# Kernel tuning notes

Hardware: AMD Instinct MI355X
Metric: run time of the kernel (lower is better)

The kernel has to match this reference:

```python
import jax, jax.numpy as jnp
import numpy as np

N = 100000           # nodes
E = 1600000          # edges (no self loops; added inside reference)
IN_DIM = 128
H1, C1 = 8, 16       # layer-1 heads, per-head channels (concat -> 128)
H2, C2 = 1, 40       # layer-2 heads, out channels (concat=False)


def setup_inputs() -> dict:
    key = jax.random.key(0)
    ks = jax.random.split(key, 10)
    x = jax.random.normal(ks[0], (N, IN_DIM), jnp.float32)
    src = jax.random.randint(ks[1], (E,), 0, N, dtype=jnp.int32)
    dst = jax.random.randint(ks[2], (E,), 0, N, dtype=jnp.int32)
    dst = jnp.where(dst == src, (dst + 1) % N, dst)  # emulate remove_self_loops
    edge_index = jnp.stack([src, dst], axis=0)
    sc = 0.05
    return {
        "x": x,
        "edge_index": edge_index,
        "W1": jax.random.normal(ks[3], (H1 * C1, IN_DIM), jnp.float32) * sc,
        "b1": jnp.zeros((H1 * C1,), jnp.float32),
        "att1": jax.random.normal(ks[4], (H1, 2 * C1), jnp.float32) * sc,
        "bias1": jnp.zeros((H1 * C1,), jnp.float32),
        "W2": jax.random.normal(ks[5], (H2 * C2, H1 * C1), jnp.float32) * sc,
        "b2": jnp.zeros((H2 * C2,), jnp.float32),
        "att2": jax.random.normal(ks[6], (H2, 2 * C2), jnp.float32) * sc,
        "bias2": jnp.zeros((C2,), jnp.float32),
    }


def _gat_layer(x, src, dst, W, b, att, bias, H, C, concat):
    n = x.shape[0]
    # add self loops (inputs are guaranteed self-loop free)
    loop = jnp.arange(n, dtype=src.dtype)
    s = jnp.concatenate([src, loop])
    d = jnp.concatenate([dst, loop])
    h = (x @ W.T + b).reshape(n, H, C)            # [N,H,C]
    # per-node halves of cat([x_i, x_j]) . att  -> gather scalars per edge
    a_i = jnp.einsum('nhc,hc->nh', h, att[:, :C])  # dst half
    a_j = jnp.einsum('nhc,hc->nh', h, att[:, C:])  # src half
    e = jax.nn.leaky_relu(a_i[d] + a_j[s], negative_slope=0.2)  # [Etot,H]
    # segment softmax over destination nodes (pyg_utils.softmax)
    m = jax.ops.segment_max(e, d, num_segments=n)
    ex = jnp.exp(e - m[d])
    denom = jax.ops.segment_sum(ex, d, num_segments=n)
    alpha = ex / (denom[d] + 1e-16)
    msg = h[s] * alpha[:, :, None]                # [Etot,H,C]
    out = jax.ops.segment_sum(msg.reshape(-1, H * C), d, num_segments=n)
    if not concat:
        out = out.reshape(n, H, C).mean(axis=1)
    return out + bias


def reference(x, edge_index, W1, b1, att1, bias1, W2, b2, att2, bias2):
    src, dst = edge_index[0], edge_index[1]
    h = _gat_layer(x, src, dst, W1, b1, att1, bias1, H1, C1, True)
    h = jax.nn.elu(h)  # dropout p=0 / eval -> no-op
    h = _gat_layer(h, src, dst, W2, b2, att2, bias2, H2, C2, False)
    return jax.nn.log_softmax(h, axis=1)
```

## Files before the change

### kernel.cpp

```cpp
#include <hip/hip_runtime.h>
#include <hip/hip_fp16.h>
#include <math.h>


typedef _Float16 f16x8 __attribute__((ext_vector_type(8)));
typedef float f32x4 __attribute__((ext_vector_type(4)));
typedef float f32x2 __attribute__((ext_vector_type(2)));

__device__ __forceinline__ float lrelu02(float x){ return x > 0.f ? x : 0.2f*x; }
__device__ __forceinline__ unsigned char f2fp8(float v){
  return (unsigned char)(__builtin_amdgcn_cvt_pk_fp8_f32(v, v, 0, false) & 0xff);
}

#define BSHIFT 7
#define BMASK  127
#define SPLIT_CHUNK 4096

__global__ void k_initcur(int* __restrict__ gcur, int nbucket, int cap){
  int b = blockIdx.x*blockDim.x + threadIdx.x;
  if (b < nbucket) gcur[b*16] = b*cap;
}

__global__ __launch_bounds__(256) void k_split(const int* __restrict__ src,
    const int* __restrict__ dst, int* __restrict__ gcur, int* __restrict__ tmp,
    int E, int nbucket){
  __shared__ int hist[1024];
  int tid = threadIdx.x;
  for (int t = tid; t < 1024; t += 256) hist[t] = 0;
  __syncthreads();
  int lo = blockIdx.x*SPLIT_CHUNK;
  int ds[16], ss[16];
  #pragma unroll
  for (int k = 0; k < 16; ++k){
    int i = lo + tid + k*256;
    bool p = i < E;
    ds[k] = p ? dst[i] : 0;
    ss[k] = p ? src[i] : 0;
    if (p) atomicAdd(&hist[ds[k] >> BSHIFT], 1);
  }
  __syncthreads();
  for (int b = tid; b < nbucket; b += 256){
    int c = hist[b];
    if (c) hist[b] = atomicAdd(&gcur[b*16], c);
  }
  __syncthreads();
  #pragma unroll
  for (int k = 0; k < 16; ++k){
    int i = lo + tid + k*256;
    if (i < E){
      int r = atomicAdd(&hist[ds[k] >> BSHIFT], 1);
      tmp[r] = ss[k] | ((ds[k] & BMASK) << 17);
    }
  }
}

__global__ void k_bscan(const int* __restrict__ gcur, int* __restrict__ bstart,
                        int* __restrict__ rowstart, int nbucket, int cap, int E, int N){
  __shared__ int lds[256];
  int t = threadIdx.x;
  int v[4]; int s = 0;
  #pragma unroll
  for (int k = 0; k < 4; ++k){
    int idx = t*4 + k;
    v[k] = (idx < nbucket) ? (gcur[idx*16] - idx*cap) : 0;
    s += v[k];
  }
  lds[t] = s;
  __syncthreads();
  for (int off = 1; off < 256; off <<= 1){
    int x = (t >= off) ? lds[t-off] : 0;
    __syncthreads();
    lds[t] += x;
    __syncthreads();
  }
  int run = (t == 0) ? 0 : lds[t-1];
  #pragma unroll
  for (int k = 0; k < 4; ++k){
    int idx = t*4 + k;
    if (idx < nbucket) bstart[idx] = run;
    run += v[k];
  }
  if (t == 0){ bstart[nbucket] = E; rowstart[N] = E; }
}

__global__ __launch_bounds__(256) void k_final(const int* __restrict__ tmp,
    const int* __restrict__ gcur, const int* __restrict__ bstart,
    int* __restrict__ rowstart, int* __restrict__ csr, int cap, int N){
  __shared__ int h[128];
  __shared__ int sc[128];
  __shared__ int cur[128];
  int b = blockIdx.x;
  int tid = threadIdx.x;
  int cnt  = gcur[b*16] - b*cap;
  int base = bstart[b];
  if (tid < 128) h[tid] = 0;
  __syncthreads();
  const int* tb = tmp + (size_t)b*cap;
  for (int i = tid; i < cnt; i += 256) atomicAdd(&h[tb[i] >> 17], 1);
  __syncthreads();
  if (tid < 128) sc[tid] = h[tid];
  __syncthreads();
  for (int off = 1; off < 128; off <<= 1){
    int x = (tid < 128 && tid >= off) ? sc[tid-off] : 0;
    __syncthreads();
    if (tid < 128) sc[tid] += x;
    __syncthreads();
  }
  if (tid < 128){
    int excl = sc[tid] - h[tid];
    int node = b*128 + tid;
    if (node < N) rowstart[node] = base + excl;
    cur[tid] = base + excl;
  }
  __syncthreads();
  for (int i = tid; i < cnt; i += 256){
    int v = tb[i];
    int p = atomicAdd(&cur[v >> 17], 1);
    csr[p] = v & 0x1FFFF;
  }
}

__global__ void k_prep(const float* __restrict__ W1, const float* __restrict__ b1,
                       const float* __restrict__ att1,
                       const float* __restrict__ W2, const float* __restrict__ b2,
                       const float* __restrict__ att2,
                       _Float16* __restrict__ W1h, _Float16* __restrict__ W2h,
                       _Float16* __restrict__ attB1, _Float16* __restrict__ attB2,
                       float* __restrict__ consts){
  int i = blockIdx.x*blockDim.x + threadIdx.x;
  if (i < 16384){ W1h[i] = (_Float16)W1[i]; return; }
  i -= 16384;
  if (i < 6144){ int r = i >> 7; W2h[i] = (r < 40)? (_Float16)W2[i] : (_Float16)0.f; return; }
  i -= 6144;
  if (i < 2048){
    int j = i >> 7, k = i & 127;
    int h = j & 7, half = (j >> 3)*16;
    float s = 0.f;
    for (int c = 0; c < 16; ++c) s += att1[h*32 + half + c]*W1[(h*16+c)*128 + k];
    attB1[i] = (_Float16)s; return;
  }
  i -= 2048;
  if (i < 2048){
    int j = i >> 7, k = i & 127;
    float s = 0.f;
    if (j < 2){ const float* av = att2 + j*40; for (int c = 0; c < 40; ++c) s += av[c]*W2[c*128 + k]; }
    attB2[i] = (_Float16)s; return;
  }
  i -= 2048;
  if (i < 18){
    float s = 0.f;
    if (i < 8){ for (int c = 0; c < 16; ++c) s += b1[i*16+c]*att1[i*32+c]; }
    else if (i < 16){ int h = i-8; for (int c = 0; c < 16; ++c) s += b1[h*16+c]*att1[h*32+16+c]; }
    else if (i == 16){ for (int c = 0; c < 40; ++c) s += b2[c]*att2[c]; }
    else { for (int c = 0; c < 40; ++c) s += b2[c]*att2[40+c]; }
    consts[i] = s;
  }
}

__global__ __launch_bounds__(256) void k_gemm1(const float* __restrict__ x,
    const _Float16* __restrict__ Wh, const _Float16* __restrict__ attB,
    const float* __restrict__ b1, const float* __restrict__ consts,
    unsigned char* __restrict__ h1f8, float* __restrict__ a1i, float* __restrict__ a1j, int N){
  int wid  = (blockIdx.x*256 + threadIdx.x) >> 6;
  int lane = threadIdx.x & 63;
  int m0 = wid*16;
  if (m0 >= N) return;
  int col = lane & 15, quad = lane >> 4;
  const float* xr = x + (size_t)(m0+col)*128 + quad*8;
  f32x4 acc[9];
  #pragma unroll
  for (int t=0;t<9;t++){ acc[t][0]=0.f; acc[t][1]=0.f; acc[t][2]=0.f; acc[t][3]=0.f; }
  #pragma unroll
  for (int q=0;q<4;q++){
    float4 f0 = ((const float4*)(xr + q*32))[0];
    float4 f1 = ((const float4*)(xr + q*32))[1];
    f16x8 a;
    a[0]=(_Float16)f0.x; a[1]=(_Float16)f0.y; a[2]=(_Float16)f0.z; a[3]=(_Float16)f0.w;
    a[4]=(_Float16)f1.x; a[5]=(_Float16)f1.y; a[6]=(_Float16)f1.z; a[7]=(_Float16)f1.w;
    #pragma unroll
    for (int t=0;t<8;t++){
      const f16x8* Bp = (const f16x8*)(Wh + (size_t)(t*16+col)*128 + q*32 + quad*8);
      acc[t] = __builtin_amdgcn_mfma_f32_16x16x32_f16(a, *Bp, acc[t], 0,0,0);
    }
    const f16x8* Ap = (const f16x8*)(attB + (size_t)col*128 + q*32 + quad*8);
    acc[8] = __builtin_amdgcn_mfma_f32_16x16x32_f16(a, *Ap, acc[8], 0,0,0);
  }
  #pragma unroll
  for (int t=0;t<8;t++){
    int c = t*16 + col;
    float bb = b1[c];
    #pragma unroll
    for (int r=0;r<4;r++){
      h1f8[(size_t)(m0 + quad*4 + r)*128 + c] = f2fp8(acc[t][r] + bb);
    }
  }
  float hb = consts[col];
  #pragma unroll
  for (int r=0;r<4;r++){
    int node = m0 + quad*4 + r;
    float v = acc[8][r] + hb;
    if (col < 8) a1i[node*8 + col] = v;
    else         a1j[node*8 + (col-8)] = v;
  }
}

__global__ __launch_bounds__(256) void k_agg1(const uint2* __restrict__ h1q,
    const float* __restrict__ a1i, const float* __restrict__ a1j,
    const int* __restrict__ rowstart, const int* __restrict__ csr,
    const float* __restrict__ bias, uint4* __restrict__ x2u4, int N){
  int lane = threadIdx.x & 63;
  int n = (blockIdx.x*blockDim.x + threadIdx.x) >> 6;
  if (n >= N) return;
  int ql = lane & 15, qt = lane >> 4;
  unsigned hd = (unsigned)ql >> 1;
  int rs = rowstart[n], re = rowstart[n+1];
  float ai2 = a1i[(unsigned)n*8u + hd];
  float a0=0.f,a1=0.f,a2=0.f,a3=0.f,a4=0.f,a5=0.f,a6=0.f,a7=0.f,den=0.f;
  {
    float w = (qt==0)? __expf(lrelu02(ai2 + a1j[(unsigned)n*8u + hd])) : 0.f;
    uint2 u = h1q[(unsigned)n*16u + (unsigned)ql];
    f32x2 f0 = __builtin_amdgcn_cvt_pk_f32_fp8((int)u.x, false);
    f32x2 f1 = __builtin_amdgcn_cvt_pk_f32_fp8((int)u.x, true);
    f32x2 f2 = __builtin_amdgcn_cvt_pk_f32_fp8((int)u.y, false);
    f32x2 f3 = __builtin_amdgcn_cvt_pk_f32_fp8((int)u.y, true);
    a0=w*f0[0]; a1=w*f0[1]; a2=w*f1[0]; a3=w*f1[1];
    a4=w*f2[0]; a5=w*f2[1]; a6=w*f3[0]; a7=w*f3[1];
    den = w;
  }
  int last = re - 1;
  if (rs < re){
    unsigned cs0 = (unsigned)csr[min(rs+ 0+qt,last)];
    unsigned cs1 = (unsigned)csr[min(rs+ 4+qt,last)];
    unsigned cs2 = (unsigned)csr[min(rs+ 8+qt,last)];
    unsigned cs3 = (unsigned)csr[min(rs+12+qt,last)];
    unsigned cs4 = (unsigned)csr[min(rs+16+qt,last)];
    unsigned cs5 = (unsigned)csr[min(rs+20+qt,last)];
    unsigned cs6 = (unsigned)csr[min(rs+24+qt,last)];
    unsigned cs7 = (unsigned)csr[min(rs+28+qt,last)];
    float aj0 = a1j[cs0*8u+hd], aj1 = a1j[cs1*8u+hd];
    float aj2 = a1j[cs2*8u+hd], aj3 = a1j[cs3*8u+hd];
    float aj4 = a1j[cs4*8u+hd], aj5 = a1j[cs5*8u+hd];
    float aj6 = a1j[cs6*8u+hd], aj7 = a1j[cs7*8u+hd];
    uint2 u0 = h1q[(size_t)cs0*16u + (unsigned)ql];
    uint2 u1 = h1q[(size_t)cs1*16u + (unsigned)ql];
    uint2 u2 = h1q[(size_t)cs2*16u + (unsigned)ql];
    uint2 u3 = h1q[(size_t)cs3*16u + (unsigned)ql];
    int e0 = rs;

#define AGG1_ST(US, CF, CS, AJ, OFF)                                         \
    {                                                                        \
      uint2 cur = US;                                                        \
      US = h1q[(size_t)CF*16u + (unsigned)ql];                               \
      unsigned nc = (unsigned)csr[min(e0+OFF+32+qt, last)];                  \
      float w = (e0+OFF+qt < re)? __expf(lrelu02(ai2 + AJ)) : 0.f;           \
      den += w;                                                              \
      f32x2 g0 = __builtin_amdgcn_cvt_pk_f32_fp8((int)cur.x, false);         \
      f32x2 g1 = __builtin_amdgcn_cvt_pk_f32_fp8((int)cur.x, true);          \
      f32x2 g2 = __builtin_amdgcn_cvt_pk_f32_fp8((int)cur.y, false);         \
      f32x2 g3 = __builtin_amdgcn_cvt_pk_f32_fp8((int)cur.y, true);          \
      a0 += w*g0[0]; a1 += w*g0[1]; a2 += w*g1[0]; a3 += w*g1[1];            \
      a4 += w*g2[0]; a5 += w*g2[1]; a6 += w*g3[0]; a7 += w*g3[1];            \
      CS = nc; AJ = a1j[nc*8u + hd];                                         \
    }

    while (e0 < re){
      AGG1_ST(u0, cs4, cs0, aj0, 0)
      if (e0+4 >= re) break;
      AGG1_ST(u1, cs5, cs1, aj1, 4)
      if (e0+8 >= re) break;
      AGG1_ST(u2, cs6, cs2, aj2, 8)
      if (e0+12 >= re) break;
      AGG1_ST(u3, cs7, cs3, aj3, 12)
      if (e0+16 >= re) break;
      AGG1_ST(u0, cs0, cs4, aj4, 16)
      if (e0+20 >= re) break;
      AGG1_ST(u1, cs1, cs5, aj5, 20)
      if (e0+24 >= re) break;
      AGG1_ST(u2, cs2, cs6, aj6, 24)
      if (e0+28 >= re) break;
      AGG1_ST(u3, cs3, cs7, aj7, 28)
      e0 += 32;
    }
#undef AGG1_ST
  }
  #pragma unroll
  for (int off = 16; off < 64; off <<= 1){
    den += __shfl_xor(den, off);
    a0 += __shfl_xor(a0, off); a1 += __shfl_xor(a1, off);
    a2 += __shfl_xor(a2, off); a3 += __shfl_xor(a3, off);
    a4 += __shfl_xor(a4, off); a5 += __shfl_xor(a5, off);
    a6 += __shfl_xor(a6, off); a7 += __shfl_xor(a7, off);
  }
  if (qt == 0){
    float invd = 1.f/(den + 1e-16f);
    const float4* b4 = (const float4*)(bias + 8*ql);
    float4 bl = b4[0], bh = b4[1];
    float o0=a0*invd+bl.x, o1=a1*invd+bl.y, o2=a2*invd+bl.z, o3=a3*invd+bl.w;
    float o4=a4*invd+bh.x, o5=a5*invd+bh.y, o6=a6*invd+bh.z, o7=a7*invd+bh.w;
    o0=(o0>0.f)?o0:(__expf(o0)-1.f); o1=(o1>0.f)?o1:(__expf(o1)-1.f);
    o2=(o2>0.f)?o2:(__expf(o2)-1.f); o3=(o3>0.f)?o3:(__expf(o3)-1.f);
    o4=(o4>0.f)?o4:(__expf(o4)-1.f); o5=(o5>0.f)?o5:(__expf(o5)-1.f);
    o6=(o6>0.f)?o6:(__expf(o6)-1.f); o7=(o7>0.f)?o7:(__expf(o7)-1.f);
    __half2 p0 = __floats2half2_rn(o0,o1), p1 = __floats2half2_rn(o2,o3);
    __half2 p2 = __floats2half2_rn(o4,o5), p3 = __floats2half2_rn(o6,o7);
    uint4 o;
    o.x = *(unsigned*)&p0; o.y = *(unsigned*)&p1; o.z = *(unsigned*)&p2; o.w = *(unsigned*)&p3;
    x2u4[(unsigned)n*16u + (unsigned)ql] = o;
  }
}

__global__ __launch_bounds__(256) void k_gemm2(const _Float16* __restrict__ xh,
    const _Float16* __restrict__ Wh, const _Float16* __restrict__ attB,
    const float* __restrict__ b2, const float* __restrict__ consts,
    unsigned char* __restrict__ h2f8, float* __restrict__ a2i, float* __restrict__ a2j, int N){
  int wid  = (blockIdx.x*256 + threadIdx.x) >> 6;
  int lane = threadIdx.x & 63;
  int m0 = wid*16;
  if (m0 >= N) return;
  int col = lane & 15, quad = lane >> 4;
  const f16x8* A8 = (const f16x8*)(xh + (size_t)(m0+col)*128 + quad*8);
  f32x4 acc[4];
  #pragma unroll
  for (int t=0;t<4;t++){ acc[t][0]=0.f; acc[t][1]=0.f; acc[t][2]=0.f; acc[t][3]=0.f; }
  #pragma unroll
  for (int q=0;q<4;q++){
    f16x8 a = A8[q*4];
    #pragma unroll
    for (int t=0;t<3;t++){
      const f16x8* Bp = (const f16x8*)(Wh + (size_t)(t*16+col)*128 + q*32 + quad*8);
      acc[t] = __builtin_amdgcn_mfma_f32_16x16x32_f16(a, *Bp, acc[t], 0,0,0);
    }
    const f16x8* Bp2 = (const f16x8*)(attB + (size_t)col*128 + q*32 + quad*8);
    acc[3] = __builtin_amdgcn_mfma_f32_16x16x32_f16(a, *Bp2, acc[3], 0,0,0);
  }
  #pragma unroll
  for (int t=0;t<3;t++){
    int c = t*16 + col;
    if (c < 40){
      float bb = b2[c];
      #pragma unroll
// ... 15 lines not shown

__global__ __launch_bounds__(256) void k_agg2(const unsigned* __restrict__ h2u,
    const float* __restrict__ a2i, const float* __restrict__ a2j,
    const int* __restrict__ rowstart, const int* __restrict__ csr,
    const float* __restrict__ bias, float* __restrict__ out, int N){
  int lane = threadIdx.x & 63;
  int wid = (blockIdx.x*blockDim.x + threadIdx.x) >> 6;
  int qt = lane >> 4, ql = lane & 15;
  int n = wid*4 + qt;
  if (n >= N) return;
  bool act = ql < 10;
  unsigned cl = act ? (unsigned)ql : 0u;
  int rs = rowstart[n], re = rowstart[n+1];
  float ai = a2i[n];
  float wself = __expf(lrelu02(ai + a2j[n]));
  float a0,a1,a2,a3,den;
  {
    unsigned u = h2u[(unsigned)n*10u + cl];
    f32x2 f0 = __builtin_amdgcn_cvt_pk_f32_fp8((int)u, false);
    f32x2 f1 = __builtin_amdgcn_cvt_pk_f32_fp8((int)u, true);
    a0 = wself*f0[0]; a1 = wself*f0[1]; a2 = wself*f1[0]; a3 = wself*f1[1];
    den = wself;
  }
  if (rs < re){
    int last = re - 1;
    unsigned cs0 = (unsigned)csr[min(rs+0,last)];
    unsigned cs1 = (unsigned)csr[min(rs+1,last)];
    unsigned cs2 = (unsigned)csr[min(rs+2,last)];
    unsigned cs3 = (unsigned)csr[min(rs+3,last)];
    unsigned cs4 = (unsigned)csr[min(rs+4,last)];
    unsigned cs5 = (unsigned)csr[min(rs+5,last)];
    unsigned cs6 = (unsigned)csr[min(rs+6,last)];
    unsigned cs7 = (unsigned)csr[min(rs+7,last)];
    float aj0 = a2j[cs0], aj1 = a2j[cs1], aj2 = a2j[cs2], aj3 = a2j[cs3];
    float aj4 = a2j[cs4], aj5 = a2j[cs5], aj6 = a2j[cs6], aj7 = a2j[cs7];
    unsigned u0 = h2u[cs0*10u + cl];
    unsigned u1 = h2u[cs1*10u + cl];
    unsigned u2 = h2u[cs2*10u + cl];
    unsigned u3 = h2u[cs3*10u + cl];
    int e0 = rs;

#define AGG2_ST(US, CF, CS, AJ, OFF)                                         \
    {                                                                        \
      unsigned cur = US;                                                     \
      US = h2u[CF*10u + cl];                                                 \
      unsigned nc = (unsigned)csr[min(e0+OFF+8, last)];                      \
      float w = (e0+OFF < re)? __expf(lrelu02(ai + AJ)) : 0.f;               \
      den += w;                                                              \
      f32x2 g0 = __builtin_amdgcn_cvt_pk_f32_fp8((int)cur, false);           \
      f32x2 g1 = __builtin_amdgcn_cvt_pk_f32_fp8((int)cur, true);            \
      a0 += w*g0[0]; a1 += w*g0[1]; a2 += w*g1[0]; a3 += w*g1[1];            \
      CS = nc; AJ = a2j[nc];                                                 \
    }

    while (e0 < re){
      AGG2_ST(u0, cs4, cs0, aj0, 0)
      AGG2_ST(u1, cs5, cs1, aj1, 1)
      AGG2_ST(u2, cs6, cs2, aj2, 2)
      AGG2_ST(u3, cs7, cs3, aj3, 3)
      AGG2_ST(u0, cs0, cs4, aj4, 4)
      AGG2_ST(u1, cs1, cs5, aj5, 5)
      AGG2_ST(u2, cs2, cs6, aj6, 6)
      AGG2_ST(u3, cs3, cs7, aj7, 7)
      e0 += 8;
    }
#undef AGG2_ST
  }
  float invd = 1.f/(den + 1e-16f);
  const float4* b4 = (const float4*)(bias + 4*cl);
  float4 bb = b4[0];
  float v0 = a0*invd + bb.x, v1 = a1*invd + bb.y;
  float v2 = a2*invd + bb.z, v3 = a3*invd + bb.w;
  float mv = act ? fmaxf(fmaxf(v0,v1), fmaxf(v2,v3)) : -INFINITY;
  #pragma unroll
  for (int off = 1; off < 16; off <<= 1) mv = fmaxf(mv, __shfl_xor(mv, off));
  float se = act ? (__expf(v0-mv)+__expf(v1-mv)+__expf(v2-mv)+__expf(v3-mv)) : 0.f;
  #pragma unroll
  for (int off = 1; off < 16; off <<= 1) se += __shfl_xor(se, off);
  float ls = __logf(se);
  if (act){
    float4 o = make_float4(v0-mv-ls, v1-mv-ls, v2-mv-ls, v3-mv-ls);
    ((float4*)out)[(unsigned)n*10u + cl] = o;
  }
}

// ... 15 lines not shown
  const int* src = ei;
  const int* dst = ei + E;

  char* ws = (char*)d_ws;
  size_t off = 0;
  auto alloc = [&](size_t bytes)->char*{
    char* p = ws + off; off += (bytes + 255) & ~(size_t)255; return p;
  };
  unsigned char* h1f8 = (unsigned char*)alloc((size_t)N*128);
  _Float16*      x2h  = (_Float16*)alloc((size_t)N*128*2);
  unsigned char* h2f8 = (unsigned char*)alloc((size_t)N*40);
  float* a1i  = (float*)alloc((size_t)N*8*4);
  float* a1j  = (float*)alloc((size_t)N*8*4);
  float* a2i  = (float*)alloc((size_t)N*4);
  float* a2j  = (float*)alloc((size_t)N*4);
  _Float16* W1h   = (_Float16*)alloc(16384*2);
  _Float16* W2h   = (_Float16*)alloc(6144*2);
  _Float16* attB1 = (_Float16*)alloc(2048*2);
  _Float16* attB2 = (_Float16*)alloc(2048*2);
  float* consts = (float*)alloc(18*4);
  int*   rowst = (int*)  alloc((size_t)(N+1)*4);
  int*   csr   = (int*)  alloc((size_t)E*4);

  int nbucket = (N + BMASK) >> BSHIFT;
  int meanb = (E + nbucket - 1)/nbucket;
  int cap = ((2*meanb + 1023)/1024)*1024;
  if (cap < 2048) cap = 2048;

  int*   gcur   = (int*)alloc((size_t)nbucket*64);
  int*   bstart = (int*)alloc((size_t)(nbucket+1)*4);
  int*   tmp    = (int*)x2h;

  int nchunk = (E + SPLIT_CHUNK - 1)/SPLIT_CHUNK;
  k_initcur<<<(nbucket+255)/256, 256, 0, stream>>>(gcur, nbucket, cap);
  k_split<<<nchunk, 256, 0, stream>>>(src, dst, gcur, tmp, E, nbucket);
  k_bscan<<<1, 256, 0, stream>>>(gcur, bstart, rowst, nbucket, cap, E, N);
  k_final<<<nbucket, 256, 0, stream>>>(tmp, gcur, bstart, rowst, csr, cap, N);
  k_prep<<<105, 256, 0, stream>>>(W1, b1, att1, W2, b2, att2, W1h, W2h, attB1, attB2, consts);

  int gblk = ((N+15)/16 + 3)/4;
  k_gemm1<<<gblk, 256, 0, stream>>>(x, W1h, attB1, b1, consts, h1f8, a1i, a1j, N);
  k_agg1<<<(N*64+255)/256, 256, 0, stream>>>((const uint2*)h1f8, a1i, a1j, rowst, csr, bias1, (uint4*)x2h, N);

  k_gemm2<<<gblk, 256, 0, stream>>>(x2h, W2h, attB2, b2, consts, h2f8, a2i, a2j, N);
  k_agg2<<<(N+15)/16, 256, 0, stream>>>((const unsigned*)h2f8, a2i, a2j, rowst, csr, bias2, (float*)d_out, N);
}
```

Measured before the change: 315.5 us.

## Fuse edge bucketing with layer-1 GEMM and widen agg1 lanes to 16 channels

The edge split (CSR bucketing) and the layer-1 GEMM now run as one horizontally fused kernel, with block index deciding which body runs. The init kernel is replaced by a memset, so bucket counters now start at zero and the bucket offset is added at use. Separately, agg1 is remapped so each lane handles 16 fp8 channels with uint4 loads and 8 edges are processed in parallel per wavefront instead of 4. This cuts launch count and lets independent work overlap, and halves gather instructions per edge. The cost is more registers per lane in agg1 and one more shuffle round in the reduction.

```diff
diff --git a/kernel.cpp b/kernel.cpp
--- a/kernel.cpp
+++ b/kernel.cpp
@@ -16,19 +16,14 @@
 #define BMASK  127
 #define SPLIT_CHUNK 4096
 
-__global__ void k_initcur(int* __restrict__ gcur, int nbucket, int cap){
-  int b = blockIdx.x*blockDim.x + threadIdx.x;
-  if (b < nbucket) gcur[b*16] = b*cap;
-}
-
-__global__ __launch_bounds__(256) void k_split(const int* __restrict__ src,
+__device__ __forceinline__ void split_body(int blk, const int* __restrict__ src,
     const int* __restrict__ dst, int* __restrict__ gcur, int* __restrict__ tmp,
-    int E, int nbucket){
+    int E, int nbucket, int cap){
   __shared__ int hist[1024];
   int tid = threadIdx.x;
   for (int t = tid; t < 1024; t += 256) hist[t] = 0;
   __syncthreads();
-  int lo = blockIdx.x*SPLIT_CHUNK;
+  int lo = blk*SPLIT_CHUNK;
   int ds[16], ss[16];
   #pragma unroll
   for (int k = 0; k < 16; ++k){
@@ -41,7 +36,7 @@
   __syncthreads();
   for (int b = tid; b < nbucket; b += 256){
     int c = hist[b];
-    if (c) hist[b] = atomicAdd(&gcur[b*16], c);
+    if (c) hist[b] = b*cap + atomicAdd(&gcur[b*16], c);
   }
   __syncthreads();
   #pragma unroll
@@ -54,15 +49,75 @@
   }
 }
 
+__device__ __forceinline__ void gemm1_body(int gb, const float* __restrict__ x,
+    const _Float16* __restrict__ Wh, const _Float16* __restrict__ attB,
+    const float* __restrict__ b1, const float* __restrict__ consts,
+    unsigned char* __restrict__ h1f8, float* __restrict__ a1i, float* __restrict__ a1j, int N){
+  int wid  = (gb*256 + (int)threadIdx.x) >> 6;
+  int lane = threadIdx.x & 63;
+  int m0 = wid*16;
+  if (m0 >= N) return;
+  int col = lane & 15, quad = lane >> 4;
+  const float* xr = x + (size_t)(m0+col)*128 + quad*8;
+  f32x4 acc[9];
+  #pragma unroll
+  for (int t=0;t<9;t++){ acc[t][0]=0.f; acc[t][1]=0.f; acc[t][2]=0.f; acc[t][3]=0.f; }
+  #pragma unroll
+  for (int q=0;q<4;q++){
+    float4 f0 = ((const float4*)(xr + q*32))[0];
+    float4 f1 = ((const float4*)(xr + q*32))[1];
+    f16x8 a;
+    a[0]=(_Float16)f0.x; a[1]=(_Float16)f0.y; a[2]=(_Float16)f0.z; a[3]=(_Float16)f0.w;
+    a[4]=(_Float16)f1.x; a[5]=(_Float16)f1.y; a[6]=(_Float16)f1.z; a[7]=(_Float16)f1.w;
+    #pragma unroll
+    for (int t=0;t<8;t++){
+      const f16x8* Bp = (const f16x8*)(Wh + (size_t)(t*16+col)*128 + q*32 + quad*8);
+      acc[t] = __builtin_amdgcn_mfma_f32_16x16x32_f16(a, *Bp, acc[t], 0,0,0);
+    }
+    const f16x8* Ap = (const f16x8*)(attB + (size_t)col*128 + q*32 + quad*8);
+    acc[8] = __builtin_amdgcn_mfma_f32_16x16x32_f16(a, *Ap, acc[8], 0,0,0);
+  }
+  #pragma unroll
+  for (int t=0;t<8;t++){
+    int c = t*16 + col;
+    float bb = b1[c];
+    #pragma unroll
+    for (int r=0;r<4;r++){
+      h1f8[(size_t)(m0 + quad*4 + r)*128 + c] = f2fp8(acc[t][r] + bb);
+    }
+  }
+  float hb = consts[col];
+  #pragma unroll
+  for (int r=0;r<4;r++){
+    int node = m0 + quad*4 + r;
+    float v = acc[8][r] + hb;
+    if (col < 8) a1i[node*8 + col] = v;
+    else         a1j[node*8 + (col-8)] = v;
+  }
+}
+
+__global__ __launch_bounds__(256) void k_fused1(const int* __restrict__ src,
+    const int* __restrict__ dst, int* __restrict__ gcur, int* __restrict__ tmp,
+    int E, int nbucket, int nchunk, int cap,
+    const float* __restrict__ x, const _Float16* __restrict__ Wh,
+    const _Float16* __restrict__ attB, const float* __restrict__ b1,
+    const float* __restrict__ consts, unsigned char* __restrict__ h1f8,
+    float* __restrict__ a1i, float* __restrict__ a1j, int N){
+  if ((int)blockIdx.x < nchunk)
+    split_body(blockIdx.x, src, dst, gcur, tmp, E, nbucket, cap);
+  else
+    gemm1_body(blockIdx.x - nchunk, x, Wh, attB, b1, consts, h1f8, a1i, a1j, N);
+}
+
 __global__ void k_bscan(const int* __restrict__ gcur, int* __restrict__ bstart,
-                        int* __restrict__ rowstart, int nbucket, int cap, int E, int N){
+                        int* __restrict__ rowstart, int nbucket, int E, int N){
   __shared__ int lds[256];
   int t = threadIdx.x;
   int v[4]; int s = 0;
   #pragma unroll
   for (int k = 0; k < 4; ++k){
     int idx = t*4 + k;
-    v[k] = (idx < nbucket) ? (gcur[idx*16] - idx*cap) : 0;
+    v[k] = (idx < nbucket) ? gcur[idx*16] : 0;
     s += v[k];
   }
   lds[t] = s;
@@ -91,7 +146,7 @@
   __shared__ int cur[128];
   int b = blockIdx.x;
   int tid = threadIdx.x;
-  int cnt  = gcur[b*16] - b*cap;
+  int cnt  = gcur[b*16];
   int base = bstart[b];
   if (tid < 128) h[tid] = 0;
   __syncthreads();
@@ -157,155 +212,126 @@
   }
 }
 
-__global__ __launch_bounds__(256) void k_gemm1(const float* __restrict__ x,
-    const _Float16* __restrict__ Wh, const _Float16* __restrict__ attB,
-    const float* __restrict__ b1, const float* __restrict__ consts,
-    unsigned char* __restrict__ h1f8, float* __restrict__ a1i, float* __restrict__ a1j, int N){
-  int wid  = (blockIdx.x*256 + threadIdx.x) >> 6;
-  int lane = threadIdx.x & 63;
-  int m0 = wid*16;
-  if (m0 >= N) return;
-  int col = lane & 15, quad = lane >> 4;
-  const float* xr = x + (size_t)(m0+col)*128 + quad*8;
-  f32x4 acc[9];
-  #pragma unroll
-  for (int t=0;t<9;t++){ acc[t][0]=0.f; acc[t][1]=0.f; acc[t][2]=0.f; acc[t][3]=0.f; }
-  #pragma unroll
-  for (int q=0;q<4;q++){
-    float4 f0 = ((const float4*)(xr + q*32))[0];
-    float4 f1 = ((const float4*)(xr + q*32))[1];
-    f16x8 a;
-    a[0]=(_Float16)f0.x; a[1]=(_Float16)f0.y; a[2]=(_Float16)f0.z; a[3]=(_Float16)f0.w;
-    a[4]=(_Float16)f1.x; a[5]=(_Float16)f1.y; a[6]=(_Float16)f1.z; a[7]=(_Float16)f1.w;
-    #pragma unroll
-    for (int t=0;t<8;t++){
-      const f16x8* Bp = (const f16x8*)(Wh + (size_t)(t*16+col)*128 + q*32 + quad*8);
-      acc[t] = __builtin_amdgcn_mfma_f32_16x16x32_f16(a, *Bp, acc[t], 0,0,0);
-    }
-    const f16x8* Ap = (const f16x8*)(attB + (size_t)col*128 + q*32 + quad*8);
-    acc[8] = __builtin_amdgcn_mfma_f32_16x16x32_f16(a, *Ap, acc[8], 0,0,0);
-  }
-  #pragma unroll
-  for (int t=0;t<8;t++){
-    int c = t*16 + col;
-    float bb = b1[c];
-    #pragma unroll
-    for (int r=0;r<4;r++){
-      h1f8[(size_t)(m0 + quad*4 + r)*128 + c] = f2fp8(acc[t][r] + bb);
-    }
-  }
-  float hb = consts[col];
-  #pragma unroll
-  for (int r=0;r<4;r++){
-    int node = m0 + quad*4 + r;
-    float v = acc[8][r] + hb;
-    if (col < 8) a1i[node*8 + col] = v;
-    else         a1j[node*8 + (col-8)] = v;
-  }
-}
-
-__global__ __launch_bounds__(256) void k_agg1(const uint2* __restrict__ h1q,
+__global__ __launch_bounds__(256) void k_agg1(const uint4* __restrict__ h1q4,
     const float* __restrict__ a1i, const float* __restrict__ a1j,
     const int* __restrict__ rowstart, const int* __restrict__ csr,
     const float* __restrict__ bias, uint4* __restrict__ x2u4, int N){
   int lane = threadIdx.x & 63;
   int n = (blockIdx.x*blockDim.x + threadIdx.x) >> 6;
   if (n >= N) return;
-  int ql = lane & 15, qt = lane >> 4;
-  unsigned hd = (unsigned)ql >> 1;
+  int o = lane & 7, oct = lane >> 3;
   int rs = rowstart[n], re = rowstart[n+1];
-  float ai2 = a1i[(unsigned)n*8u + hd];
-  float a0=0.f,a1=0.f,a2=0.f,a3=0.f,a4=0.f,a5=0.f,a6=0.f,a7=0.f,den=0.f;
+  float ai2 = a1i[(unsigned)n*8u + (unsigned)o];
+  float s0=0.f,s1=0.f,s2=0.f,s3=0.f,s4=0.f,s5=0.f,s6=0.f,s7=0.f;
+  float s8=0.f,s9=0.f,s10=0.f,s11=0.f,s12=0.f,s13=0.f,s14=0.f,s15=0.f;
+  float den=0.f;
+
+#define ACC16(U, W)                                                          \
+  { f32x2 g;                                                                 \
+    g = __builtin_amdgcn_cvt_pk_f32_fp8((int)(U).x,false); s0 +=(W)*g[0]; s1 +=(W)*g[1]; \
+    g = __builtin_amdgcn_cvt_pk_f32_fp8((int)(U).x,true ); s2 +=(W)*g[0]; s3 +=(W)*g[1]; \
+    g = __builtin_amdgcn_cvt_pk_f32_fp8((int)(U).y,false); s4 +=(W)*g[0]; s5 +=(W)*g[1]; \
+    g = __builtin_amdgcn_cvt_pk_f32_fp8((int)(U).y,true ); s6 +=(W)*g[0]; s7 +=(W)*g[1]; \
+    g = __builtin_amdgcn_cvt_pk_f32_fp8((int)(U).z,false); s8 +=(W)*g[0]; s9 +=(W)*g[1]; \
+    g = __builtin_amdgcn_cvt_pk_f32_fp8((int)(U).z,true ); s10+=(W)*g[0]; s11+=(W)*g[1]; \
+    g = __builtin_amdgcn_cvt_pk_f32_fp8((int)(U).w,false); s12+=(W)*g[0]; s13+=(W)*g[1]; \
+    g = __builtin_amdgcn_cvt_pk_f32_fp8((int)(U).w,true ); s14+=(W)*g[0]; s15+=(W)*g[1]; }
+
   {
-    float w = (qt==0)? __expf(lrelu02(ai2 + a1j[(unsigned)n*8u + hd])) : 0.f;
-    uint2 u = h1q[(unsigned)n*16u + (unsigned)ql];
-    f32x2 f0 = __builtin_amdgcn_cvt_pk_f32_fp8((int)u.x, false);
-    f32x2 f1 = __builtin_amdgcn_cvt_pk_f32_fp8((int)u.x, true);
-    f32x2 f2 = __builtin_amdgcn_cvt_pk_f32_fp8((int)u.y, false);
-    f32x2 f3 = __builtin_amdgcn_cvt_pk_f32_fp8((int)u.y, true);
-    a0=w*f0[0]; a1=w*f0[1]; a2=w*f1[0]; a3=w*f1[1];
-    a4=w*f2[0]; a5=w*f2[1]; a6=w*f3[0]; a7=w*f3[1];
+    float w = (oct==0)? __expf(lrelu02(ai2 + a1j[(unsigned)n*8u + (unsigned)o])) : 0.f;
+    uint4 u = h1q4[(unsigned)n*8u + (unsigned)o];
+    ACC16(u, w)
     den = w;
   }
   int last = re - 1;
   if (rs < re){
-    unsigned cs0 = (unsigned)csr[min(rs+ 0+qt,last)];
-    unsigned cs1 = (unsigned)csr[min(rs+ 4+qt,last)];
-    unsigned cs2 = (unsigned)csr[min(rs+ 8+qt,last)];
-    unsigned cs3 = (unsigned)csr[min(rs+12+qt,last)];
-    unsigned cs4 = (unsigned)csr[min(rs+16+qt,last)];
-    unsigned cs5 = (unsigned)csr[min(rs+20+qt,last)];
-    unsigned cs6 = (unsigned)csr[min(rs+24+qt,last)];
-    unsigned cs7 = (unsigned)csr[min(rs+28+qt,last)];
-    float aj0 = a1j[cs0*8u+hd], aj1 = a1j[cs1*8u+hd];
-    float aj2 = a1j[cs2*8u+hd], aj3 = a1j[cs3*8u+hd];
-    float aj4 = a1j[cs4*8u+hd], aj5 = a1j[cs5*8u+hd];
-    float aj6 = a1j[cs6*8u+hd], aj7 = a1j[cs7*8u+hd];
-    uint2 u0 = h1q[(size_t)cs0*16u + (unsigned)ql];
-    uint2 u1 = h1q[(size_t)cs1*16u + (unsigned)ql];
-    uint2 u2 = h1q[(size_t)cs2*16u + (unsigned)ql];
-    uint2 u3 = h1q[(size_t)cs3*16u + (unsigned)ql];
+    unsigned cs0 = (unsigned)csr[min(rs+ 0+oct,last)];
+    unsigned cs1 = (unsigned)csr[min(rs+ 8+oct,last)];
+    unsigned cs2 = (unsigned)csr[min(rs+16+oct,last)];
+    unsigned cs3 = (unsigned)csr[min(rs+24+oct,last)];
+    unsigned cs4 = (unsigned)csr[min(rs+32+oct,last)];
+    unsigned cs5 = (unsigned)csr[min(rs+40+oct,last)];
+    unsigned cs6 = (unsigned)csr[min(rs+48+oct,last)];
+    unsigned cs7 = (unsigned)csr[min(rs+56+oct,last)];
+    float aj0 = a1j[cs0*8u+o], aj1 = a1j[cs1*8u+o];
+    float aj2 = a1j[cs2*8u+o], aj3 = a1j[cs3*8u+o];
+    float aj4 = a1j[cs4*8u+o], aj5 = a1j[cs5*8u+o];
+    float aj6 = a1j[cs6*8u+o], aj7 = a1j[cs7*8u+o];
+    uint4 u0 = h1q4[(size_t)cs0*8u + (unsigned)o];
+    uint4 u1 = h1q4[(size_t)cs1*8u + (unsigned)o];
+    uint4 u2 = h1q4[(size_t)cs2*8u + (unsigned)o];
+    uint4 u3 = h1q4[(size_t)cs3*8u + (unsigned)o];
     int e0 = rs;
 
 #define AGG1_ST(US, CF, CS, AJ, OFF)                                         \
     {                                                                        \
-      uint2 cur = US;                                                        \
-      US = h1q[(size_t)CF*16u + (unsigned)ql];                               \
-      unsigned nc = (unsigned)csr[min(e0+OFF+32+qt, last)];                  \
-      float w = (e0+OFF+qt < re)? __expf(lrelu02(ai2 + AJ)) : 0.f;           \
+      uint4 cur = US;                                                        \
+      US = h1q4[(size_t)CF*8u + (unsigned)o];                                \
+      unsigned nc = (unsigned)csr[min(e0+OFF+64+oct, last)];                 \
+      float w = (e0+OFF+oct < re)? __expf(lrelu02(ai2 + AJ)) : 0.f;          \
       den += w;                                                              \
-      f32x2 g0 = __builtin_amdgcn_cvt_pk_f32_fp8((int)cur.x, false);         \
-      f32x2 g1 = __builtin_amdgcn_cvt_pk_f32_fp8((int)cur.x, true);          \
-      f32x2 g2 = __builtin_amdgcn_cvt_pk_f32_fp8((int)cur.y, false);         \
-      f32x2 g3 = __builtin_amdgcn_cvt_pk_f32_fp8((int)cur.y, true);          \
-      a0 += w*g0[0]; a1 += w*g0[1]; a2 += w*g1[0]; a3 += w*g1[1];            \
-      a4 += w*g2[0]; a5 += w*g2[1]; a6 += w*g3[0]; a7 += w*g3[1];            \
-      CS = nc; AJ = a1j[nc*8u + hd];                                         \
+      ACC16(cur, w)                                                          \
+      CS = nc; AJ = a1j[nc*8u + (unsigned)o];                                \
     }
 
     while (e0 < re){
       AGG1_ST(u0, cs4, cs0, aj0, 0)
-      if (e0+4 >= re) break;
-      AGG1_ST(u1, cs5, cs1, aj1, 4)
       if (e0+8 >= re) break;
-      AGG1_ST(u2, cs6, cs2, aj2, 8)
-      if (e0+12 >= re) break;
-      AGG1_ST(u3, cs7, cs3, aj3, 12)
+      AGG1_ST(u1, cs5, cs1, aj1, 8)
       if (e0+16 >= re) break;
-      AGG1_ST(u0, cs0, cs4, aj4, 16)
-      if (e0+20 >= re) break;
-      AGG1_ST(u1, cs1, cs5, aj5, 20)
+      AGG1_ST(u2, cs6, cs2, aj2, 16)
       if (e0+24 >= re) break;
-      AGG1_ST(u2, cs2, cs6, aj6, 24)
-      if (e0+28 >= re) break;
-      AGG1_ST(u3, cs3, cs7, aj7, 28)
-      e0 += 32;
+      AGG1_ST(u3, cs7, cs3, aj3, 24)
+      if (e0+32 >= re) break;
+      AGG1_ST(u0, cs0, cs4, aj4, 32)
+      if (e0+40 >= re) break;
+      AGG1_ST(u1, cs1, cs5, aj5, 40)
+      if (e0+48 >= re) break;
+      AGG1_ST(u2, cs2, cs6, aj6, 48)
+      if (e0+56 >= re) break;
+      AGG1_ST(u3, cs3, cs7, aj7, 56)
+      e0 += 64;
     }
 #undef AGG1_ST
   }
-  #pragma unroll
-  for (int off = 16; off < 64; off <<= 1){
+#undef ACC16
+  #pragma unroll
+  for (int off = 8; off < 64; off <<= 1){
     den += __shfl_xor(den, off);
-    a0 += __shfl_xor(a0, off); a1 += __shfl_xor(a1, off);
-    a2 += __shfl_xor(a2, off); a3 += __shfl_xor(a3, off);
-    a4 += __shfl_xor(a4, off); a5 += __shfl_xor(a5, off);
-    a6 += __shfl_xor(a6, off); a7 += __shfl_xor(a7, off);
-  }
-  if (qt == 0){
+    s0 += __shfl_xor(s0, off);  s1 += __shfl_xor(s1, off);
+    s2 += __shfl_xor(s2, off);  s3 += __shfl_xor(s3, off);
+    s4 += __shfl_xor(s4, off);  s5 += __shfl_xor(s5, off);
+    s6 += __shfl_xor(s6, off);  s7 += __shfl_xor(s7, off);
+    s8 += __shfl_xor(s8, off);  s9 += __shfl_xor(s9, off);
+    s10+= __shfl_xor(s10,off);  s11+= __shfl_xor(s11,off);
+    s12+= __shfl_xor(s12,off);  s13+= __shfl_xor(s13,off);
+    s14+= __shfl_xor(s14,off);  s15+= __shfl_xor(s15,off);
+  }
+  if (oct == 0){
     float invd = 1.f/(den + 1e-16f);
-    const float4* b4 = (const float4*)(bias + 8*ql);
-    float4 bl = b4[0], bh = b4[1];
-    float o0=a0*invd+bl.x, o1=a1*invd+bl.y, o2=a2*invd+bl.z, o3=a3*invd+bl.w;
-    float o4=a4*invd+bh.x, o5=a5*invd+bh.y, o6=a6*invd+bh.z, o7=a7*invd+bh.w;
-    o0=(o0>0.f)?o0:(__expf(o0)-1.f); o1=(o1>0.f)?o1:(__expf(o1)-1.f);
-    o2=(o2>0.f)?o2:(__expf(o2)-1.f); o3=(o3>0.f)?o3:(__expf(o3)-1.f);
-    o4=(o4>0.f)?o4:(__expf(o4)-1.f); o5=(o5>0.f)?o5:(__expf(o5)-1.f);
-    o6=(o6>0.f)?o6:(__expf(o6)-1.f); o7=(o7>0.f)?o7:(__expf(o7)-1.f);
-    __half2 p0 = __floats2half2_rn(o0,o1), p1 = __floats2half2_rn(o2,o3);
-    __half2 p2 = __floats2half2_rn(o4,o5), p3 = __floats2half2_rn(o6,o7);
-    uint4 o;
-    o.x = *(unsigned*)&p0; o.y = *(unsigned*)&p1; o.z = *(unsigned*)&p2; o.w = *(unsigned*)&p3;
-    x2u4[(unsigned)n*16u + (unsigned)ql] = o;
+    const float4* b4 = (const float4*)(bias + 16*o);
+    float4 bb0 = b4[0], bb1 = b4[1], bb2 = b4[2], bb3 = b4[3];
+    float o0 =s0 *invd+bb0.x, o1 =s1 *invd+bb0.y, o2 =s2 *invd+bb0.z, o3 =s3 *invd+bb0.w;
+    float o4 =s4 *invd+bb1.x, o5 =s5 *invd+bb1.y, o6 =s6 *invd+bb1.z, o7 =s7 *invd+bb1.w;
+    float o8 =s8 *invd+bb2.x, o9 =s9 *invd+bb2.y, o10=s10*invd+bb2.z, o11=s11*invd+bb2.w;
+    float o12=s12*invd+bb3.x, o13=s13*invd+bb3.y, o14=s14*invd+bb3.z, o15=s15*invd+bb3.w;
+    o0 =(o0 >0.f)?o0 :(__expf(o0 )-1.f); o1 =(o1 >0.f)?o1 :(__expf(o1 )-1.f);
+    o2 =(o2 >0.f)?o2 :(__expf(o2 )-1.f); o3 =(o3 >0.f)?o3 :(__expf(o3 )-1.f);
+    o4 =(o4 >0.f)?o4 :(__expf(o4 )-1.f); o5 =(o5 >0.f)?o5 :(__expf(o5 )-1.f);
+    o6 =(o6 >0.f)?o6 :(__expf(o6 )-1.f); o7 =(o7 >0.f)?o7 :(__expf(o7 )-1.f);
+    o8 =(o8 >0.f)?o8 :(__expf(o8 )-1.f); o9 =(o9 >0.f)?o9 :(__expf(o9 )-1.f);
+    o10=(o10>0.f)?o10:(__expf(o10)-1.f); o11=(o11>0.f)?o11:(__expf(o11)-1.f);
+    o12=(o12>0.f)?o12:(__expf(o12)-1.f); o13=(o13>0.f)?o13:(__expf(o13)-1.f);
+    o14=(o14>0.f)?o14:(__expf(o14)-1.f); o15=(o15>0.f)?o15:(__expf(o15)-1.f);
+    __half2 p0 = __floats2half2_rn(o0 ,o1 ), p1 = __floats2half2_rn(o2 ,o3 );
+    __half2 p2 = __floats2half2_rn(o4 ,o5 ), p3 = __floats2half2_rn(o6 ,o7 );
+    __half2 p4 = __floats2half2_rn(o8 ,o9 ), p5 = __floats2half2_rn(o10,o11);
+    __half2 p6 = __floats2half2_rn(o12,o13), p7 = __floats2half2_rn(o14,o15);
+    uint4 w0, w1;
+    w0.x = *(unsigned*)&p0; w0.y = *(unsigned*)&p1; w0.z = *(unsigned*)&p2; w0.w = *(unsigned*)&p3;
+    w1.x = *(unsigned*)&p4; w1.y = *(unsigned*)&p5; w1.z = *(unsigned*)&p6; w1.w = *(unsigned*)&p7;
+    x2u4[(unsigned)n*16u + (unsigned)(o*2)    ] = w0;
+    x2u4[(unsigned)n*16u + (unsigned)(o*2 + 1)] = w1;
   }
 }
 
@@ -487,15 +513,16 @@
   int*   tmp    = (int*)x2h;
 
   int nchunk = (E + SPLIT_CHUNK - 1)/SPLIT_CHUNK;
-  k_initcur<<<(nbucket+255)/256, 256, 0, stream>>>(gcur, nbucket, cap);
-  k_split<<<nchunk, 256, 0, stream>>>(src, dst, gcur, tmp, E, nbucket);
-  k_bscan<<<1, 256, 0, stream>>>(gcur, bstart, rowst, nbucket, cap, E, N);
+  int gblk = ((N+15)/16 + 3)/4;
+
+  hipMemsetAsync(gcur, 0, (size_t)nbucket*64, stream);
+  k_prep<<<105, 256, 0, stream>>>(W1, b1, att1, W2, b2, att2, W1h, W2h, attB1, attB2, consts);
+  k_fused1<<<nchunk + gblk, 256, 0, stream>>>(src, dst, gcur, tmp, E, nbucket, nchunk, cap,
+                                              x, W1h, attB1, b1, consts, h1f8, a1i, a1j, N);
+  k_bscan<<<1, 256, 0, stream>>>(gcur, bstart, rowst, nbucket, E, N);
   k_final<<<nbucket, 256, 0, stream>>>(tmp, gcur, bstart, rowst, csr, cap, N);
-  k_prep<<<105, 256, 0, stream>>>(W1, b1, att1, W2, b2, att2, W1h, W2h, attB1, attB2, consts);
-
-  int gblk = ((N+15)/16 + 3)/4;
-  k_gemm1<<<gblk, 256, 0, stream>>>(x, W1h, attB1, b1, consts, h1f8, a1i, a1j, N);
-  k_agg1<<<(N*64+255)/256, 256, 0, stream>>>((const uint2*)h1f8, a1i, a1j, rowst, csr, bias1, (uint4*)x2h, N);
+
+  k_agg1<<<(N*64+255)/256, 256, 0, stream>>>((const uint4*)h1f8, a1i, a1j, rowst, csr, bias1, (uint4*)x2h, N);
 
   k_gemm2<<<gblk, 256, 0, stream>>>(x2h, W2h, attB2, b2, consts, h2f8, a2i, a2j, N);
   k_agg2<<<(N+15)/16, 256, 0, stream>>>((const unsigned*)h2f8, a2i, a2j, rowst, csr, bias2, (float*)d_out, N);
```

Result: faster. 303.3 us (-3.9%).

## Fuse edge bucketing with layer-1 GEMM in one launch and simplify agg masks

Applied to the files above, without the earlier changes.

Merges the edge-split kernel and the layer-1 GEMM into a single launch with disjoint block ranges, so the independent CSR bucketing and the dense projection run concurrently. Counters now start at zero via hipMemsetAsync, which removes the init kernel, and the bucket offset is added per use. In the aggregation loops, out-of-range edges get -INF attention logits when loaded, which removes the per-edge bounds test before exp. Some index arithmetic moves from 64-bit to 32-bit. The fused kernel mixes two very different workloads, which may affect occupancy and register allocation for the split blocks.

```diff
diff --git a/kernel.cpp b/kernel.cpp
--- a/kernel.cpp
+++ b/kernel.cpp
@@ -16,19 +16,14 @@
 #define BMASK  127
 #define SPLIT_CHUNK 4096
 
-__global__ void k_initcur(int* __restrict__ gcur, int nbucket, int cap){
-  int b = blockIdx.x*blockDim.x + threadIdx.x;
-  if (b < nbucket) gcur[b*16] = b*cap;
-}
-
-__global__ __launch_bounds__(256) void k_split(const int* __restrict__ src,
+__device__ __forceinline__ void split_body(int blk, const int* __restrict__ src,
     const int* __restrict__ dst, int* __restrict__ gcur, int* __restrict__ tmp,
-    int E, int nbucket){
+    int E, int nbucket, int cap){
   __shared__ int hist[1024];
   int tid = threadIdx.x;
   for (int t = tid; t < 1024; t += 256) hist[t] = 0;
   __syncthreads();
-  int lo = blockIdx.x*SPLIT_CHUNK;
+  int lo = blk*SPLIT_CHUNK;
   int ds[16], ss[16];
   #pragma unroll
   for (int k = 0; k < 16; ++k){
@@ -41,7 +36,7 @@
   __syncthreads();
   for (int b = tid; b < nbucket; b += 256){
     int c = hist[b];
-    if (c) hist[b] = atomicAdd(&gcur[b*16], c);
+    if (c) hist[b] = b*cap + atomicAdd(&gcur[b*16], c);
   }
   __syncthreads();
   #pragma unroll
@@ -54,15 +49,75 @@
   }
 }
 
+__device__ __forceinline__ void gemm1_body(int gb, const float* __restrict__ x,
+    const _Float16* __restrict__ Wh, const _Float16* __restrict__ attB,
+    const float* __restrict__ b1, const float* __restrict__ consts,
+    unsigned char* __restrict__ h1f8, float* __restrict__ a1i, float* __restrict__ a1j, int N){
+  int wid  = (gb*256 + (int)threadIdx.x) >> 6;
+  int lane = threadIdx.x & 63;
+  int m0 = wid*16;
+  if (m0 >= N) return;
+  int col = lane & 15, quad = lane >> 4;
+  const float* xr = x + (size_t)(m0+col)*128 + quad*8;
+  f32x4 acc[9];
+  #pragma unroll
+  for (int t=0;t<9;t++){ acc[t][0]=0.f; acc[t][1]=0.f; acc[t][2]=0.f; acc[t][3]=0.f; }
+  #pragma unroll
+  for (int q=0;q<4;q++){
+    float4 f0 = ((const float4*)(xr + q*32))[0];
+    float4 f1 = ((const float4*)(xr + q*32))[1];
+    f16x8 a;
+    a[0]=(_Float16)f0.x; a[1]=(_Float16)f0.y; a[2]=(_Float16)f0.z; a[3]=(_Float16)f0.w;
+    a[4]=(_Float16)f1.x; a[5]=(_Float16)f1.y; a[6]=(_Float16)f1.z; a[7]=(_Float16)f1.w;
+    #pragma unroll
+    for (int t=0;t<8;t++){
+      const f16x8* Bp = (const f16x8*)(Wh + (size_t)(t*16+col)*128 + q*32 + quad*8);
+      acc[t] = __builtin_amdgcn_mfma_f32_16x16x32_f16(a, *Bp, acc[t], 0,0,0);
+    }
+    const f16x8* Ap = (const f16x8*)(attB + (size_t)col*128 + q*32 + quad*8);
+    acc[8] = __builtin_amdgcn_mfma_f32_16x16x32_f16(a, *Ap, acc[8], 0,0,0);
+  }
+  #pragma unroll
+  for (int t=0;t<8;t++){
+    int c = t*16 + col;
+    float bb = b1[c];
+    #pragma unroll
+    for (int r=0;r<4;r++){
+      h1f8[(size_t)(m0 + quad*4 + r)*128 + c] = f2fp8(acc[t][r] + bb);
+    }
+  }
+  float hb = consts[col];
+  #pragma unroll
+  for (int r=0;r<4;r++){
+    int node = m0 + quad*4 + r;
+    float v = acc[8][r] + hb;
+    if (col < 8) a1i[node*8 + col] = v;
+    else         a1j[node*8 + (col-8)] = v;
+  }
+}
+
+__global__ __launch_bounds__(256) void k_fused1(const int* __restrict__ src,
+    const int* __restrict__ dst, int* __restrict__ gcur, int* __restrict__ tmp,
+    int E, int nbucket, int nchunk, int cap,
+    const float* __restrict__ x, const _Float16* __restrict__ Wh,
+    const _Float16* __restrict__ attB, const float* __restrict__ b1,
+    const float* __restrict__ consts, unsigned char* __restrict__ h1f8,
+    float* __restrict__ a1i, float* __restrict__ a1j, int N){
+  if ((int)blockIdx.x < nchunk)
+    split_body(blockIdx.x, src, dst, gcur, tmp, E, nbucket, cap);
+  else
+    gemm1_body(blockIdx.x - nchunk, x, Wh, attB, b1, consts, h1f8, a1i, a1j, N);
+}
+
 __global__ void k_bscan(const int* __restrict__ gcur, int* __restrict__ bstart,
-                        int* __restrict__ rowstart, int nbucket, int cap, int E, int N){
+                        int* __restrict__ rowstart, int nbucket, int E, int N){
   __shared__ int lds[256];
   int t = threadIdx.x;
   int v[4]; int s = 0;
   #pragma unroll
   for (int k = 0; k < 4; ++k){
     int idx = t*4 + k;
-    v[k] = (idx < nbucket) ? (gcur[idx*16] - idx*cap) : 0;
+    v[k] = (idx < nbucket) ? gcur[idx*16] : 0;
     s += v[k];
   }
   lds[t] = s;
@@ -91,7 +146,7 @@
   __shared__ int cur[128];
   int b = blockIdx.x;
   int tid = threadIdx.x;
-  int cnt  = gcur[b*16] - b*cap;
+  int cnt  = gcur[b*16];
   int base = bstart[b];
   if (tid < 128) h[tid] = 0;
   __syncthreads();
@@ -157,53 +212,6 @@
   }
 }
 
-__global__ __launch_bounds__(256) void k_gemm1(const float* __restrict__ x,
-    const _Float16* __restrict__ Wh, const _Float16* __restrict__ attB,
-    const float* __restrict__ b1, const float* __restrict__ consts,
-    unsigned char* __restrict__ h1f8, float* __restrict__ a1i, float* __restrict__ a1j, int N){
-  int wid  = (blockIdx.x*256 + threadIdx.x) >> 6;
-  int lane = threadIdx.x & 63;
-  int m0 = wid*16;
-  if (m0 >= N) return;
-  int col = lane & 15, quad = lane >> 4;
-  const float* xr = x + (size_t)(m0+col)*128 + quad*8;
-  f32x4 acc[9];
-  #pragma unroll
-  for (int t=0;t<9;t++){ acc[t][0]=0.f; acc[t][1]=0.f; acc[t][2]=0.f; acc[t][3]=0.f; }
-  #pragma unroll
-  for (int q=0;q<4;q++){
-    float4 f0 = ((const float4*)(xr + q*32))[0];
-    float4 f1 = ((const float4*)(xr + q*32))[1];
-    f16x8 a;
-    a[0]=(_Float16)f0.x; a[1]=(_Float16)f0.y; a[2]=(_Float16)f0.z; a[3]=(_Float16)f0.w;
-    a[4]=(_Float16)f1.x; a[5]=(_Float16)f1.y; a[6]=(_Float16)f1.z; a[7]=(_Float16)f1.w;
-    #pragma unroll
-    for (int t=0;t<8;t++){
-      const f16x8* Bp = (const f16x8*)(Wh + (size_t)(t*16+col)*128 + q*32 + quad*8);
-      acc[t] = __builtin_amdgcn_mfma_f32_16x16x32_f16(a, *Bp, acc[t], 0,0,0);
-    }
-    const f16x8* Ap = (const f16x8*)(attB + (size_t)col*128 + q*32 + quad*8);
-    acc[8] = __builtin_amdgcn_mfma_f32_16x16x32_f16(a, *Ap, acc[8], 0,0,0);
-  }
-  #pragma unroll
-  for (int t=0;t<8;t++){
-    int c = t*16 + col;
-    float bb = b1[c];
-    #pragma unroll
-    for (int r=0;r<4;r++){
-      h1f8[(size_t)(m0 + quad*4 + r)*128 + c] = f2fp8(acc[t][r] + bb);
-    }
-  }
-  float hb = consts[col];
-  #pragma unroll
-  for (int r=0;r<4;r++){
-    int node = m0 + quad*4 + r;
-    float v = acc[8][r] + hb;
-    if (col < 8) a1i[node*8 + col] = v;
-    else         a1j[node*8 + (col-8)] = v;
-  }
-}
-
 __global__ __launch_bounds__(256) void k_agg1(const uint2* __restrict__ h1q,
     const float* __restrict__ a1i, const float* __restrict__ a1j,
     const int* __restrict__ rowstart, const int* __restrict__ csr,
@@ -211,14 +219,15 @@
   int lane = threadIdx.x & 63;
   int n = (blockIdx.x*blockDim.x + threadIdx.x) >> 6;
   if (n >= N) return;
-  int ql = lane & 15, qt = lane >> 4;
-  unsigned hd = (unsigned)ql >> 1;
+  unsigned ql = lane & 15;
+  int qt = lane >> 4;
+  unsigned hd = ql >> 1;
   int rs = rowstart[n], re = rowstart[n+1];
   float ai2 = a1i[(unsigned)n*8u + hd];
   float a0=0.f,a1=0.f,a2=0.f,a3=0.f,a4=0.f,a5=0.f,a6=0.f,a7=0.f,den=0.f;
   {
     float w = (qt==0)? __expf(lrelu02(ai2 + a1j[(unsigned)n*8u + hd])) : 0.f;
-    uint2 u = h1q[(unsigned)n*16u + (unsigned)ql];
+    uint2 u = h1q[(unsigned)n*16u + ql];
     f32x2 f0 = __builtin_amdgcn_cvt_pk_f32_fp8((int)u.x, false);
     f32x2 f1 = __builtin_amdgcn_cvt_pk_f32_fp8((int)u.x, true);
     f32x2 f2 = __builtin_amdgcn_cvt_pk_f32_fp8((int)u.y, false);
@@ -237,22 +246,27 @@
     unsigned cs5 = (unsigned)csr[min(rs+20+qt,last)];
     unsigned cs6 = (unsigned)csr[min(rs+24+qt,last)];
     unsigned cs7 = (unsigned)csr[min(rs+28+qt,last)];
-    float aj0 = a1j[cs0*8u+hd], aj1 = a1j[cs1*8u+hd];
-    float aj2 = a1j[cs2*8u+hd], aj3 = a1j[cs3*8u+hd];
-    float aj4 = a1j[cs4*8u+hd], aj5 = a1j[cs5*8u+hd];
-    float aj6 = a1j[cs6*8u+hd], aj7 = a1j[cs7*8u+hd];
-    uint2 u0 = h1q[(size_t)cs0*16u + (unsigned)ql];
-    uint2 u1 = h1q[(size_t)cs1*16u + (unsigned)ql];
-    uint2 u2 = h1q[(size_t)cs2*16u + (unsigned)ql];
-    uint2 u3 = h1q[(size_t)cs3*16u + (unsigned)ql];
+    float aj0 = (rs+ 0+qt < re)? a1j[cs0*8u+hd] : -INFINITY;
+    float aj1 = (rs+ 4+qt < re)? a1j[cs1*8u+hd] : -INFINITY;
+    float aj2 = (rs+ 8+qt < re)? a1j[cs2*8u+hd] : -INFINITY;
+    float aj3 = (rs+12+qt < re)? a1j[cs3*8u+hd] : -INFINITY;
+    float aj4 = (rs+16+qt < re)? a1j[cs4*8u+hd] : -INFINITY;
+    float aj5 = (rs+20+qt < re)? a1j[cs5*8u+hd] : -INFINITY;
+    float aj6 = (rs+24+qt < re)? a1j[cs6*8u+hd] : -INFINITY;
+    float aj7 = (rs+28+qt < re)? a1j[cs7*8u+hd] : -INFINITY;
+    uint2 u0 = h1q[cs0*16u + ql];
+    uint2 u1 = h1q[cs1*16u + ql];
+    uint2 u2 = h1q[cs2*16u + ql];
+    uint2 u3 = h1q[cs3*16u + ql];
     int e0 = rs;
 
 #define AGG1_ST(US, CF, CS, AJ, OFF)                                         \
     {                                                                        \
       uint2 cur = US;                                                        \
-      US = h1q[(size_t)CF*16u + (unsigned)ql];                               \
-      unsigned nc = (unsigned)csr[min(e0+OFF+32+qt, last)];                  \
-      float w = (e0+OFF+qt < re)? __expf(lrelu02(ai2 + AJ)) : 0.f;           \
+      US = h1q[CF*16u + ql];                                                 \
+      int idx = e0+OFF+32+qt;                                                \
+      unsigned nc = (unsigned)csr[min(idx, last)];                           \
+      float w = __expf(lrelu02(ai2 + AJ));                                   \
       den += w;                                                              \
       f32x2 g0 = __builtin_amdgcn_cvt_pk_f32_fp8((int)cur.x, false);         \
       f32x2 g1 = __builtin_amdgcn_cvt_pk_f32_fp8((int)cur.x, true);          \
@@ -260,7 +274,7 @@
       f32x2 g3 = __builtin_amdgcn_cvt_pk_f32_fp8((int)cur.y, true);          \
       a0 += w*g0[0]; a1 += w*g0[1]; a2 += w*g1[0]; a3 += w*g1[1];            \
       a4 += w*g2[0]; a5 += w*g2[1]; a6 += w*g3[0]; a7 += w*g3[1];            \
-      CS = nc; AJ = a1j[nc*8u + hd];                                         \
+      CS = nc; AJ = (idx < re)? a1j[nc*8u + hd] : -INFINITY;                 \
     }
 
     while (e0 < re){
@@ -305,7 +319,7 @@
     __half2 p2 = __floats2half2_rn(o4,o5), p3 = __floats2half2_rn(o6,o7);
     uint4 o;
     o.x = *(unsigned*)&p0; o.y = *(unsigned*)&p1; o.z = *(unsigned*)&p2; o.w = *(unsigned*)&p3;
-    x2u4[(unsigned)n*16u + (unsigned)ql] = o;
+    x2u4[(unsigned)n*16u + ql] = o;
   }
 }
 
@@ -387,8 +401,14 @@
     unsigned cs5 = (unsigned)csr[min(rs+5,last)];
     unsigned cs6 = (unsigned)csr[min(rs+6,last)];
     unsigned cs7 = (unsigned)csr[min(rs+7,last)];
-    float aj0 = a2j[cs0], aj1 = a2j[cs1], aj2 = a2j[cs2], aj3 = a2j[cs3];
-    float aj4 = a2j[cs4], aj5 = a2j[cs5], aj6 = a2j[cs6], aj7 = a2j[cs7];
+    float aj0 = (rs+0 < re)? a2j[cs0] : -INFINITY;
+    float aj1 = (rs+1 < re)? a2j[cs1] : -INFINITY;
+    float aj2 = (rs+2 < re)? a2j[cs2] : -INFINITY;
+    float aj3 = (rs+3 < re)? a2j[cs3] : -INFINITY;
+    float aj4 = (rs+4 < re)? a2j[cs4] : -INFINITY;
+    float aj5 = (rs+5 < re)? a2j[cs5] : -INFINITY;
+    float aj6 = (rs+6 < re)? a2j[cs6] : -INFINITY;
+    float aj7 = (rs+7 < re)? a2j[cs7] : -INFINITY;
     unsigned u0 = h2u[cs0*10u + cl];
     unsigned u1 = h2u[cs1*10u + cl];
     unsigned u2 = h2u[cs2*10u + cl];
@@ -399,13 +419,14 @@
     {                                                                        \
       unsigned cur = US;                                                     \
       US = h2u[CF*10u + cl];                                                 \
-      unsigned nc = (unsigned)csr[min(e0+OFF+8, last)];                      \
-      float w = (e0+OFF < re)? __expf(lrelu02(ai + AJ)) : 0.f;               \
+      int idx = e0+OFF+8;                                                    \
+      unsigned nc = (unsigned)csr[min(idx, last)];                           \
+      float w = __expf(lrelu02(ai + AJ));                                    \
       den += w;                                                              \
       f32x2 g0 = __builtin_amdgcn_cvt_pk_f32_fp8((int)cur, false);           \
       f32x2 g1 = __builtin_amdgcn_cvt_pk_f32_fp8((int)cur, true);            \
       a0 += w*g0[0]; a1 += w*g0[1]; a2 += w*g1[0]; a3 += w*g1[1];            \
-      CS = nc; AJ = a2j[nc];                                                 \
+      CS = nc; AJ = (idx < re)? a2j[nc] : -INFINITY;                         \
     }
 
     while (e0 < re){
@@ -487,14 +508,15 @@
   int*   tmp    = (int*)x2h;
 
   int nchunk = (E + SPLIT_CHUNK - 1)/SPLIT_CHUNK;
-  k_initcur<<<(nbucket+255)/256, 256, 0, stream>>>(gcur, nbucket, cap);
-  k_split<<<nchunk, 256, 0, stream>>>(src, dst, gcur, tmp, E, nbucket);
-  k_bscan<<<1, 256, 0, stream>>>(gcur, bstart, rowst, nbucket, cap, E, N);
+  int gblk = ((N+15)/16 + 3)/4;
+
+  hipMemsetAsync(gcur, 0, (size_t)nbucket*64, stream);
+  k_prep<<<105, 256, 0, stream>>>(W1, b1, att1, W2, b2, att2, W1h, W2h, attB1, attB2, consts);
+  k_fused1<<<nchunk + gblk, 256, 0, stream>>>(src, dst, gcur, tmp, E, nbucket, nchunk, cap,
+                                              x, W1h, attB1, b1, consts, h1f8, a1i, a1j, N);
+  k_bscan<<<1, 256, 0, stream>>>(gcur, bstart, rowst, nbucket, E, N);
   k_final<<<nbucket, 256, 0, stream>>>(tmp, gcur, bstart, rowst, csr, cap, N);
-  k_prep<<<105, 256, 0, stream>>>(W1, b1, att1, W2, b2, att2, W1h, W2h, attB1, attB2, consts);
-
-  int gblk = ((N+15)/16 + 3)/4;
-  k_gemm1<<<gblk, 256, 0, stream>>>(x, W1h, attB1, b1, consts, h1f8, a1i, a1j, N);
+
   k_agg1<<<(N*64+255)/256, 256, 0, stream>>>((const uint2*)h1f8, a1i, a1j, rowst, csr, bias1, (uint4*)x2h, N);
 
   k_gemm2<<<gblk, 256, 0, stream>>>(x2h, W2h, attB2, b2, consts, h2f8, a2i, a2j, N);
```

Measured after the change: 306.7 us. 2.8% less time.
